# Performance work log

Measured on AMD Instinct MI355X. Metric: run time of the kernel, lower is better.

## Reference

```python
import jax, jax.numpy as jnp
import numpy as np

EMBED_DIM = 1024
HEADS = 16
HEAD_DIM = EMBED_DIM // HEADS


def setup_inputs() -> dict:
    key = jax.random.key(0)
    ks = jax.random.split(key, 9)
    B, T, C = 4, 4096, EMBED_DIM
    s = 1.0 / np.sqrt(C)
    inp = {
        "x": jax.random.normal(ks[0], (B, T, C), dtype=jnp.float32),
        "Wq": jax.random.normal(ks[1], (C, C), dtype=jnp.float32) * s,
        "bq": jnp.zeros((C,), dtype=jnp.float32),
        "Wk": jax.random.normal(ks[2], (C, C), dtype=jnp.float32) * s,
        "bk": jnp.zeros((C,), dtype=jnp.float32),
        "Wv": jax.random.normal(ks[3], (C, C), dtype=jnp.float32) * s,
        "bv": jnp.zeros((C,), dtype=jnp.float32),
        "Wc": jax.random.normal(ks[4], (C, C), dtype=jnp.float32) * s,
        "bc": jnp.zeros((C,), dtype=jnp.float32),
    }
    return inp


def reference(x, Wq, bq, Wk, bk, Wv, bv, Wc, bc):
    B, T, C = x.shape
    H, D = HEADS, HEAD_DIM
    # projections (torch Linear: x @ W.T + b)
    q = (x @ Wq.T + bq).reshape(B, T, H, D).transpose(0, 2, 1, 3)  # [B,H,T,D]
    k = (x @ Wk.T + bk).reshape(B, T, H, D).transpose(0, 2, 1, 3)
    v = (x @ Wv.T + bv).reshape(B, T, H, D).transpose(0, 2, 1, 3)
    # ELU+1 feature map
    q = jax.nn.elu(q) + 1.0
    k = jax.nn.elu(k) + 1.0
    # kv outer product: [B,H,D,D]
    kv = jnp.einsum("bhtd,bhte->bhde", k, v)
    # normalizer: q @ sum_t k  -> [B,H,T,1]
    k_sum = k.sum(axis=2)  # [B,H,D]
    z = 1.0 / (jnp.einsum("bhtd,bhd->bht", q, k_sum)[..., None] + 1e-6)
    y = jnp.einsum("bhtd,bhde->bhte", q, kv) * z  # [B,H,T,D]
    y = y.transpose(0, 2, 1, 3).reshape(B, T, C)
    return y @ Wc.T + bc
```

## Files before the change

### kernel.cpp

```cpp
#include <hip/hip_runtime.h>
#include <math.h>

#define EMBED 1024
#define HEADS 16
#define HD 64
#define BATCH 4
#define TSEQ 4096
#define BH (BATCH * HEADS)
#define MROWS (BATCH * TSEQ)

typedef _Float16 f16;
typedef __attribute__((ext_vector_type(4))) _Float16 f16x4;
typedef __attribute__((ext_vector_type(8))) _Float16 f16x8;
typedef __attribute__((ext_vector_type(4))) float f32x4;

#define GLOBAL_AS __attribute__((address_space(1)))
#define LDS_AS __attribute__((address_space(3)))

__device__ __forceinline__ float elu1(float v) {
    return v > 0.f ? v + 1.f : __expf(v);
}

__device__ __forceinline__ int swzc(int row, int col, int cols) {
    int g = (col >> 3) ^ (row & 7);
    return row * cols + (g << 3) + (col & 7);
}

__device__ __forceinline__ f16x8 fragld(const f16* t, int row, int k, int cols) {
    return *(const f16x8*)&t[swzc(row, k, cols)];
}

__device__ __forceinline__ f32x4 mfma16(f16x8 a, f16x8 b, f32x4 c) {
    return __builtin_amdgcn_mfma_f32_16x16x32_f16(a, b, c, 0, 0, 0);
}

__device__ __forceinline__ void gld_lds16(const f16* g, f16* l) {
    __builtin_amdgcn_global_load_lds((const GLOBAL_AS void*)g, (LDS_AS void*)l, 16, 0, 0);
}

__global__ __launch_bounds__(256) void prep(
    const float* __restrict__ x, f16* __restrict__ xh,
    const float* __restrict__ Wq, const float* __restrict__ Wk,
    const float* __restrict__ Wv, const float* __restrict__ Wc,
    const float* __restrict__ bq, const float* __restrict__ bk,
    const float* __restrict__ bv, const float* __restrict__ bc,
    f16* __restrict__ Wall, float* __restrict__ ball, float* __restrict__ kvz)
{
    int bid = blockIdx.x;
    if (bid < 16384) {
        size_t i4 = (size_t)bid * 256 + threadIdx.x;
        float4 f = *(const float4*)&x[i4 * 4];
        f16x4 h = {(f16)f.x, (f16)f.y, (f16)f.z, (f16)f.w};
        *(f16x4*)&xh[i4 * 4] = h;
    } else {
        int i4 = (bid - 16384) * 256 + threadIdx.x;
        int cls = i4 >> 18;
        const float* W = cls == 0 ? Wq : cls == 1 ? Wk : cls == 2 ? Wv : Wc;
        int off = (i4 & 0x3FFFF) * 4;
        float4 f = *(const float4*)&W[off];
        f16x4 h = {(f16)f.x, (f16)f.y, (f16)f.z, (f16)f.w};
        *(f16x4*)&Wall[(size_t)i4 * 4] = h;
        if (i4 < 4096) {
            int c2 = i4 >> 10;
            const float* bb = c2 == 0 ? bq : c2 == 1 ? bk : c2 == 2 ? bv : bc;
            ball[i4] = bb[i4 & 1023];
        }
        if (i4 < 66560) {
            *(float4*)&kvz[i4 * 4] = (float4){0.f, 0.f, 0.f, 0.f};
        }
    }
}

__global__ __launch_bounds__(256) void gemm_qkv(
    const f16* __restrict__ xh, const f16* __restrict__ Wall,
    const float* __restrict__ ball,
    f16* __restrict__ q, float* __restrict__ kvg, float* __restrict__ ksg)
{
    __shared__ __align__(16) f16 smem[2 * 128 * 64];
    f16* As = smem;
    f16* Bs = smem + 128 * 64;

    const int tid = threadIdx.x, lane = tid & 63, w = tid >> 6;
    const int wr = w >> 1, wc4 = w & 1, l15 = lane & 15, l4 = lane >> 4;

    const int m0 = blockIdx.x * 128;
    const int ny = blockIdx.y;
    const bool isq = (ny < 8);
    const int h = ny - 8;

    const int gcol = ((lane & 7) ^ (lane >> 3)) << 3;
    const int rsub = lane >> 3;
    const size_t arow = (size_t)(m0 + w * 32 + rsub) * EMBED + gcol;

    const int wrow = w * 32 + rsub;
    int brow_idx;
    if (isq)          brow_idx = ny * 128 + wrow;
    else if (wrow < 64) brow_idx = 1024 + h * 64 + wrow;
    else                brow_idx = 2048 + h * 64 + (wrow - 64);
    const size_t brow = (size_t)brow_idx * EMBED + gcol;

    f32x4 acc[4][4];
    #pragma unroll
    for (int i = 0; i < 4; ++i)
        #pragma unroll
        for (int j = 0; j < 4; ++j) acc[i][j] = (f32x4){0.f, 0.f, 0.f, 0.f};

    for (int k0 = 0; k0 < EMBED; k0 += 64) {
        #pragma unroll
        for (int c = 0; c < 4; ++c) {
            gld_lds16(&xh[arow + (size_t)c * 8 * EMBED + k0], &As[(w * 4 + c) * 512]);
            gld_lds16(&Wall[brow + (size_t)c * 8 * EMBED + k0], &Bs[(w * 4 + c) * 512]);
        }
        __syncthreads();
        #pragma unroll
        for (int kk = 0; kk < 64; kk += 32) {
            f16x8 af[4], bf[4];
            #pragma unroll
            for (int i = 0; i < 4; ++i)
                af[i] = fragld(As, wr * 64 + i * 16 + l15, kk + l4 * 8, 64);
            #pragma unroll
            for (int j = 0; j < 4; ++j)
                bf[j] = fragld(Bs, wc4 * 64 + j * 16 + l15, kk + l4 * 8, 64);
            #pragma unroll
            for (int i = 0; i < 4; ++i)
                #pragma unroll
                for (int j = 0; j < 4; ++j)
                    acc[i][j] = mfma16(af[i], bf[j], acc[i][j]);
        }
        __syncthreads();
    }

    if (isq) {
        const int n0 = ny * 128;
        #pragma unroll
        for (int j = 0; j < 4; ++j) {
            int c = wc4 * 64 + j * 16 + l15;
            float bj = ball[n0 + c];
            #pragma unroll
            for (int i = 0; i < 4; ++i) {
                #pragma unroll
                for (int r = 0; r < 4; ++r) {
                    int t = wr * 64 + i * 16 + l4 * 4 + r;
                    smem[swzc(t, c, 128)] = (f16)elu1(acc[i][j][r] + bj);
                }
            }
        }
        __syncthreads();
        #pragma unroll
        for (int p = 0; p < 8; ++p) {
            int idx = tid + p * 256;
            int row = idx >> 4, g8 = (idx & 15) << 3;
            f16x8 v = *(const f16x8*)&smem[swzc(row, g8, 128)];
            *(f16x8*)&q[(size_t)(m0 + row) * EMBED + n0 + g8] = v;
        }
    } else {
        f16* kt = As;
        f16* vt = Bs;
        const float* biasp = ball + (wc4 ? 2048 : 1024) + h * 64;
        #pragma unroll
        for (int j = 0; j < 4; ++j) {
            int d = j * 16 + l15;
            float bj = biasp[d];
            f16* dst = wc4 ? vt : kt;
            #pragma unroll
            for (int i = 0; i < 4; ++i) {
                int t0 = wr * 64 + i * 16 + l4 * 4;
                f16x4 hv;
                #pragma unroll
                for (int r = 0; r < 4; ++r) {
                    float vv = acc[i][j][r] + bj;
                    if (!wc4) vv = elu1(vv);
                    hv[r] = (f16)vv;
                }
                *(f16x4*)&dst[swzc(d, t0, 128)] = hv;
            }
        }
        __syncthreads();

        f32x4 kvacc[4];
        #pragma unroll
        for (int j = 0; j < 4; ++j) kvacc[j] = (f32x4){0.f, 0.f, 0.f, 0.f};
        #pragma unroll
        for (int tc = 0; tc < 4; ++tc) {
            f16x8 a = fragld(vt, 16 * w + l15, tc * 32 + l4 * 8, 128);
            #pragma unroll
            for (int j = 0; j < 4; ++j) {
                f16x8 bfr = fragld(kt, j * 16 + l15, tc * 32 + l4 * 8, 128);
                kvacc[j] = mfma16(a, bfr, kvacc[j]);
            }
        }
        float ksacc = 0.f;
        {
            int d = tid & 63, q4 = tid >> 6;
            #pragma unroll
            for (int t8 = 0; t8 < 32; t8 += 8) {
                f16x8 k8 = fragld(kt, d, q4 * 32 + t8, 128);
                #pragma unroll
                for (int e = 0; e < 8; ++e) ksacc += (float)k8[e];
            }
        }
        const int bh = (m0 >> 12) * HEADS + h;
        #pragma unroll
        for (int j = 0; j < 4; ++j)
            #pragma unroll
            for (int r = 0; r < 4; ++r)
                atomicAdd(&kvg[(size_t)bh * 4096 +
                               (size_t)(16 * w + l4 * 4 + r) * HD + j * 16 + l15],
                          kvacc[j][r]);
        atomicAdd(&ksg[bh * HD + (tid & 63)], ksacc);
    }
}

__global__ __launch_bounds__(256) void y_kernel(
    const f16* __restrict__ q, const float* __restrict__ kvg,
    const float* __restrict__ ksg, f16* __restrict__ y)
{
    __shared__ __align__(16) f16 qs[128 * 64];
    __shared__ __align__(16) f16 kvs[64 * 64];
    __shared__ __align__(16) f16 ylds[128 * 64];
    __shared__ float kss[64];
    __shared__ float zs[128];

    const int bh = blockIdx.x, b = bh >> 4, h = bh & 15;
    const int tid = threadIdx.x, lane = tid & 63, w = tid >> 6;
    const int l15 = lane & 15, l4 = lane >> 4;
    const int t0g = b * TSEQ + blockIdx.y * 128;

    #pragma unroll
    for (int c = 0; c < 4; ++c) {
        int idx = tid + c * 256;
        int row = idx >> 3, col8 = (idx & 7) << 3;
        f16x8 v = *(const f16x8*)&q[(size_t)(t0g + row) * EMBED + h * 64 + col8];
        *(f16x8*)&qs[swzc(row, col8, 64)] = v;
    }
    #pragma unroll
    for (int c = 0; c < 4; ++c) {
        int idx = tid + c * 256;
        int e = idx >> 4, d4 = (idx & 15) << 2;
        float4 f = *(const float4*)&kvg[(size_t)bh * 4096 + e * 64 + d4];
        f16x4 hv = {(f16)f.x, (f16)f.y, (f16)f.z, (f16)f.w};
        *(f16x4*)&kvs[swzc(e, d4, 64)] = hv;
    }
    if (tid < 64) kss[tid] = ksg[bh * HD + tid];
    __syncthreads();

    {
        int t = tid >> 1, dh = (tid & 1) * 32;
        float s = 0.f;
        #pragma unroll
        for (int d8 = 0; d8 < 32; d8 += 8) {
            f16x8 qv = fragld(qs, t, dh + d8, 64);
            #pragma unroll
            for (int e = 0; e < 8; ++e) s += (float)qv[e] * kss[dh + d8 + e];
        }
        s += __shfl_xor(s, 1);
        if ((tid & 1) == 0) zs[t] = 1.f / (s + 1e-6f);
    }
    __syncthreads();

    f32x4 yacc[8];
    #pragma unroll
    for (int jn = 0; jn < 8; ++jn) yacc[jn] = (f32x4){0.f, 0.f, 0.f, 0.f};
    #pragma unroll
    for (int kk = 0; kk < 64; kk += 32) {
        f16x8 a = fragld(kvs, 16 * w + l15, kk + l4 * 8, 64);
        #pragma unroll
        for (int jn = 0; jn < 8; ++jn) {
            f16x8 bq8 = fragld(qs, jn * 16 + l15, kk + l4 * 8, 64);
            yacc[jn] = mfma16(a, bq8, yacc[jn]);
        }
    }
    #pragma unroll
    for (int jn = 0; jn < 8; ++jn) {
        int t = jn * 16 + l15;
        float z = zs[t];
        int e0 = 16 * w + l4 * 4;
        f16x4 hv;
        #pragma unroll
        for (int r = 0; r < 4; ++r) hv[r] = (f16)(yacc[jn][r] * z);
        *(f16x4*)&ylds[swzc(t, e0, 64)] = hv;
    }
    __syncthreads();

    {
        int row = tid >> 1, eh = (tid & 1) * 32;
        size_t gb = (size_t)(t0g + row) * EMBED + h * 64 + eh;
        #pragma unroll
        for (int c8 = 0; c8 < 32; c8 += 8) {
            f16x8 v = fragld(ylds, row, eh + c8, 64);
            *(f16x8*)&y[gb + c8] = v;
        }
    }
}

__global__ __launch_bounds__(256) void gemm_out(
    const f16* __restrict__ y, const f16* __restrict__ Wall,
    const float* __restrict__ ball, float* __restrict__ out)
{
    __shared__ __align__(16) f16 As[128 * 64];
    __shared__ __align__(16) f16 Bs[128 * 64];

    const int tid = threadIdx.x, lane = tid & 63, w = tid >> 6;
    const int wr = w >> 1, wc4 = w & 1, l15 = lane & 15, l4 = lane >> 4;
    const int m0 = blockIdx.x * 128;
    const int n0 = blockIdx.y * 128;

    const int gcol = ((lane & 7) ^ (lane >> 3)) << 3;
    const int rsub = lane >> 3;
    const size_t arow = (size_t)(m0 + w * 32 + rsub) * EMBED + gcol;
    const size_t brow = (size_t)(3072 + n0 + w * 32 + rsub) * EMBED + gcol;

    f32x4 acc[4][4];
    #pragma unroll
    for (int i = 0; i < 4; ++i)
        #pragma unroll
        for (int j = 0; j < 4; ++j) acc[i][j] = (f32x4){0.f, 0.f, 0.f, 0.f};

    for (int k0 = 0; k0 < EMBED; k0 += 64) {
        #pragma unroll
        for (int c = 0; c < 4; ++c) {
            gld_lds16(&y[arow + (size_t)c * 8 * EMBED + k0], &As[(w * 4 + c) * 512]);
            gld_lds16(&Wall[brow + (size_t)c * 8 * EMBED + k0], &Bs[(w * 4 + c) * 512]);
        }
        __syncthreads();
        #pragma unroll
        for (int kk = 0; kk < 64; kk += 32) {
            f16x8 af[4], bf[4];
            #pragma unroll
            for (int i = 0; i < 4; ++i)
                af[i] = fragld(As, wr * 64 + i * 16 + l15, kk + l4 * 8, 64);
            #pragma unroll
            for (int j = 0; j < 4; ++j)
                bf[j] = fragld(Bs, wc4 * 64 + j * 16 + l15, kk + l4 * 8, 64);
            #pragma unroll
            for (int i = 0; i < 4; ++i)
                #pragma unroll
                for (int j = 0; j < 4; ++j)
                    acc[i][j] = mfma16(af[i], bf[j], acc[i][j]);
        }
        __syncthreads();
    }

    #pragma unroll
    for (int j = 0; j < 4; ++j) {
        int n = n0 + wc4 * 64 + j * 16 + l15;
        float bj = ball[3072 + n];
        #pragma unroll
        for (int i = 0; i < 4; ++i) {
            #pragma unroll
            for (int r = 0; r < 4; ++r) {
                int m = m0 + wr * 64 + i * 16 + l4 * 4 + r;
                out[(size_t)m * EMBED + n] = acc[i][j][r] + bj;
            }
        }
    }
}

extern "C" void kernel_launch(void* const* d_in, const int* in_sizes, int n_in,
                              void* d_out, int out_size, void* d_ws, size_t ws_size,
                              hipStream_t stream) {
    (void)in_sizes; (void)n_in; (void)out_size; (void)ws_size;
    const float* x  = (const float*)d_in[0];
    const float* Wq = (const float*)d_in[1];
    const float* bq = (const float*)d_in[2];
    const float* Wk = (const float*)d_in[3];
    const float* bk = (const float*)d_in[4];
    const float* Wv = (const float*)d_in[5];
    const float* bv = (const float*)d_in[6];
    const float* Wc = (const float*)d_in[7];
    const float* bc = (const float*)d_in[8];
    float* out = (float*)d_out;

    char* W = (char*)d_ws;
    f16* xh   = (f16*)W;
    f16* q_ws = (f16*)(W + 33554432);
    f16* Wall = (f16*)(W + 67108864);
    float* ball = (float*)(W + 75497472);
    float* kvg  = (float*)(W + 75513856);
    float* ksg  = (float*)(W + 76562432);

    prep<<<20480, 256, 0, stream>>>(x, xh, Wq, Wk, Wv, Wc, bq, bk, bv, bc,
                                    Wall, ball, kvg);

    gemm_qkv<<<dim3(128, 24), 256, 0, stream>>>(xh, Wall, ball, q_ws, kvg, ksg);

    y_kernel<<<dim3(BH, TSEQ / 128), 256, 0, stream>>>(q_ws, kvg, ksg, q_ws);

    gemm_out<<<dim3(128, 8), 256, 0, stream>>>(q_ws, Wall, ball, out);
}
```

Baseline: 226.2 us.

## Split KV projection from Q projection and fuse Q GEMM with y computation

The combined QKV GEMM becomes two kernels. The first computes only K/V and accumulates kv and k_sum with atomics. The second computes the Q projection tile and then applies ELU+1, the normalizer and the kv product in the epilogue for the two heads covered by each 128-column tile, writing y directly. This removes the q round-trip through global memory and the separate y_kernel launch. In exchange the Q GEMM now must wait until all K/V work finishes, and the fused epilogue adds LDS traffic and register pressure.

```diff
diff --git a/kernel.cpp b/kernel.cpp
--- a/kernel.cpp
+++ b/kernel.cpp
@@ -71,10 +71,10 @@
     }
 }
 
-__global__ __launch_bounds__(256) void gemm_qkv(
+__global__ __launch_bounds__(256) void gemm_kv(
     const f16* __restrict__ xh, const f16* __restrict__ Wall,
     const float* __restrict__ ball,
-    f16* __restrict__ q, float* __restrict__ kvg, float* __restrict__ ksg)
+    float* __restrict__ kvg, float* __restrict__ ksg)
 {
     __shared__ __align__(16) f16 smem[2 * 128 * 64];
     f16* As = smem;
@@ -84,19 +84,15 @@
     const int wr = w >> 1, wc4 = w & 1, l15 = lane & 15, l4 = lane >> 4;
 
     const int m0 = blockIdx.x * 128;
-    const int ny = blockIdx.y;
-    const bool isq = (ny < 8);
-    const int h = ny - 8;
+    const int h = blockIdx.y;
 
     const int gcol = ((lane & 7) ^ (lane >> 3)) << 3;
     const int rsub = lane >> 3;
     const size_t arow = (size_t)(m0 + w * 32 + rsub) * EMBED + gcol;
 
     const int wrow = w * 32 + rsub;
-    int brow_idx;
-    if (isq)          brow_idx = ny * 128 + wrow;
-    else if (wrow < 64) brow_idx = 1024 + h * 64 + wrow;
-    else                brow_idx = 2048 + h * 64 + (wrow - 64);
+    const int brow_idx = (wrow < 64) ? (1024 + h * 64 + wrow)
+                                     : (2048 + h * 64 + (wrow - 64));
     const size_t brow = (size_t)brow_idx * EMBED + gcol;
 
     f32x4 acc[4][4];
@@ -130,166 +126,199 @@
         __syncthreads();
     }
 
-    if (isq) {
-        const int n0 = ny * 128;
+    f16* kt = As;
+    f16* vt = Bs;
+    const float* biasp = ball + (wc4 ? 2048 : 1024) + h * 64;
+    #pragma unroll
+    for (int j = 0; j < 4; ++j) {
+        int d = j * 16 + l15;
+        float bj = biasp[d];
+        f16* dst = wc4 ? vt : kt;
+        #pragma unroll
+        for (int i = 0; i < 4; ++i) {
+            int t0 = wr * 64 + i * 16 + l4 * 4;
+            f16x4 hv;
+            #pragma unroll
+            for (int r = 0; r < 4; ++r) {
+                float vv = acc[i][j][r] + bj;
+                if (!wc4) vv = elu1(vv);
+                hv[r] = (f16)vv;
+            }
+            *(f16x4*)&dst[swzc(d, t0, 128)] = hv;
+        }
+    }
+    __syncthreads();
+
+    f32x4 kvacc[4];
+    #pragma unroll
+    for (int j = 0; j < 4; ++j) kvacc[j] = (f32x4){0.f, 0.f, 0.f, 0.f};
+    #pragma unroll
+    for (int tc = 0; tc < 4; ++tc) {
+        f16x8 a = fragld(vt, 16 * w + l15, tc * 32 + l4 * 8, 128);
         #pragma unroll
         for (int j = 0; j < 4; ++j) {
-            int c = wc4 * 64 + j * 16 + l15;
-            float bj = ball[n0 + c];
-            #pragma unroll
-            for (int i = 0; i < 4; ++i) {
+            f16x8 bfr = fragld(kt, j * 16 + l15, tc * 32 + l4 * 8, 128);
+            kvacc[j] = mfma16(a, bfr, kvacc[j]);
+        }
+    }
+    float ksacc = 0.f;
+    {
+        int d = tid & 63, q4 = tid >> 6;
+        #pragma unroll
+        for (int t8 = 0; t8 < 32; t8 += 8) {
+            f16x8 k8 = fragld(kt, d, q4 * 32 + t8, 128);
+            #pragma unroll
+            for (int e = 0; e < 8; ++e) ksacc += (float)k8[e];
+        }
+    }
+    const int bh = (m0 >> 12) * HEADS + h;
+    #pragma unroll
+    for (int j = 0; j < 4; ++j)
+        #pragma unroll
+        for (int r = 0; r < 4; ++r)
+            atomicAdd(&kvg[(size_t)bh * 4096 +
+                           (size_t)(16 * w + l4 * 4 + r) * HD + j * 16 + l15],
+                      kvacc[j][r]);
+    atomicAdd(&ksg[bh * HD + (tid & 63)], ksacc);
+}
+
+__global__ __launch_bounds__(256) void gemm_qy(
+    const f16* __restrict__ xh, const f16* __restrict__ Wall,
+    const float* __restrict__ ball,
+    const float* __restrict__ kvg, const float* __restrict__ ksg,
+    f16* __restrict__ y)
+{
+    __shared__ __align__(16) f16 smem[2 * 128 * 64];
+    __shared__ __align__(16) f16 kvs[2][64 * 64];
+    __shared__ float kss[2][64];
+    __shared__ float zs[128][2];
+    f16* As = smem;
+    f16* Bs = smem + 128 * 64;
+
+    const int tid = threadIdx.x, lane = tid & 63, w = tid >> 6;
+    const int wr = w >> 1, wc4 = w & 1, l15 = lane & 15, l4 = lane >> 4;
+
+    const int m0 = blockIdx.x * 128;
+    const int ny = blockIdx.y;
+    const int n0 = ny * 128;
+    const int bh0 = (m0 >> 12) * HEADS + 2 * ny;
+
+    const int gcol = ((lane & 7) ^ (lane >> 3)) << 3;
+    const int rsub = lane >> 3;
+    const size_t arow = (size_t)(m0 + w * 32 + rsub) * EMBED + gcol;
+    const size_t brow = (size_t)(n0 + w * 32 + rsub) * EMBED + gcol;
+
+    f32x4 acc[4][4];
+    #pragma unroll
+    for (int i = 0; i < 4; ++i)
+        #pragma unroll
+        for (int j = 0; j < 4; ++j) acc[i][j] = (f32x4){0.f, 0.f, 0.f, 0.f};
+
+    for (int k0 = 0; k0 < EMBED; k0 += 64) {
+        #pragma unroll
+        for (int c = 0; c < 4; ++c) {
+            gld_lds16(&xh[arow + (size_t)c * 8 * EMBED + k0], &As[(w * 4 + c) * 512]);
+            gld_lds16(&Wall[brow + (size_t)c * 8 * EMBED + k0], &Bs[(w * 4 + c) * 512]);
+        }
+        __syncthreads();
+        #pragma unroll
+        for (int kk = 0; kk < 64; kk += 32) {
+            f16x8 af[4], bf[4];
+            #pragma unroll
+            for (int i = 0; i < 4; ++i)
+                af[i] = fragld(As, wr * 64 + i * 16 + l15, kk + l4 * 8, 64);
+            #pragma unroll
+            for (int j = 0; j < 4; ++j)
+                bf[j] = fragld(Bs, wc4 * 64 + j * 16 + l15, kk + l4 * 8, 64);
+            #pragma unroll
+            for (int i = 0; i < 4; ++i)
                 #pragma unroll
-                for (int r = 0; r < 4; ++r) {
-                    int t = wr * 64 + i * 16 + l4 * 4 + r;
-                    smem[swzc(t, c, 128)] = (f16)elu1(acc[i][j][r] + bj);
-                }
+                for (int j = 0; j < 4; ++j)
+                    acc[i][j] = mfma16(af[i], bf[j], acc[i][j]);
+        }
+        __syncthreads();
+    }
+
+    #pragma unroll
+    for (int c = 0; c < 8; ++c) {
+        int idx = tid + c * 256;
+        int hh = idx >> 10;
+        int rem = idx & 1023;
+        int e = rem >> 4, d4 = (rem & 15) << 2;
+        float4 f = *(const float4*)&kvg[(size_t)(bh0 + hh) * 4096 + e * 64 + d4];
+        f16x4 hv = {(f16)f.x, (f16)f.y, (f16)f.z, (f16)f.w};
+        *(f16x4*)&kvs[hh][swzc(e, d4, 64)] = hv;
+    }
+    if (tid < 128) kss[tid >> 6][tid & 63] = ksg[(bh0 + (tid >> 6)) * HD + (tid & 63)];
+
+    #pragma unroll
+    for (int j = 0; j < 4; ++j) {
+        int c = wc4 * 64 + j * 16 + l15;
+        float bj = ball[n0 + c];
+        #pragma unroll
+        for (int i = 0; i < 4; ++i) {
+            #pragma unroll
+            for (int r = 0; r < 4; ++r) {
+                int t = wr * 64 + i * 16 + l4 * 4 + r;
+                smem[swzc(t, c, 128)] = (f16)elu1(acc[i][j][r] + bj);
             }
         }
-        __syncthreads();
-        #pragma unroll
-        for (int p = 0; p < 8; ++p) {
-            int idx = tid + p * 256;
-            int row = idx >> 4, g8 = (idx & 15) << 3;
-            f16x8 v = *(const f16x8*)&smem[swzc(row, g8, 128)];
-            *(f16x8*)&q[(size_t)(m0 + row) * EMBED + n0 + g8] = v;
-        }
-    } else {
-        f16* kt = As;
-        f16* vt = Bs;
-        const float* biasp = ball + (wc4 ? 2048 : 1024) + h * 64;
-        #pragma unroll
-        for (int j = 0; j < 4; ++j) {
-            int d = j * 16 + l15;
-            float bj = biasp[d];
-            f16* dst = wc4 ? vt : kt;
-            #pragma unroll
-            for (int i = 0; i < 4; ++i) {
-                int t0 = wr * 64 + i * 16 + l4 * 4;
-                f16x4 hv;
-                #pragma unroll
-                for (int r = 0; r < 4; ++r) {
-                    float vv = acc[i][j][r] + bj;
-                    if (!wc4) vv = elu1(vv);
-                    hv[r] = (f16)vv;
-                }
-                *(f16x4*)&dst[swzc(d, t0, 128)] = hv;
-            }
-        }
-        __syncthreads();
-
-        f32x4 kvacc[4];
-        #pragma unroll
-        for (int j = 0; j < 4; ++j) kvacc[j] = (f32x4){0.f, 0.f, 0.f, 0.f};
-        #pragma unroll
-        for (int tc = 0; tc < 4; ++tc) {
-            f16x8 a = fragld(vt, 16 * w + l15, tc * 32 + l4 * 8, 128);
-            #pragma unroll
-            for (int j = 0; j < 4; ++j) {
-                f16x8 bfr = fragld(kt, j * 16 + l15, tc * 32 + l4 * 8, 128);
-                kvacc[j] = mfma16(a, bfr, kvacc[j]);
-            }
-        }
-        float ksacc = 0.f;
-        {
-            int d = tid & 63, q4 = tid >> 6;
-            #pragma unroll
-            for (int t8 = 0; t8 < 32; t8 += 8) {
-                f16x8 k8 = fragld(kt, d, q4 * 32 + t8, 128);
-                #pragma unroll
-                for (int e = 0; e < 8; ++e) ksacc += (float)k8[e];
-            }
-        }
-        const int bh = (m0 >> 12) * HEADS + h;
-        #pragma unroll
-        for (int j = 0; j < 4; ++j)
-            #pragma unroll
-            for (int r = 0; r < 4; ++r)
-                atomicAdd(&kvg[(size_t)bh * 4096 +
-                               (size_t)(16 * w + l4 * 4 + r) * HD + j * 16 + l15],
-                          kvacc[j][r]);
-        atomicAdd(&ksg[bh * HD + (tid & 63)], ksacc);
-    }
-}
-
-__global__ __launch_bounds__(256) void y_kernel(
-    const f16* __restrict__ q, const float* __restrict__ kvg,
-    const float* __restrict__ ksg, f16* __restrict__ y)
-{
-    __shared__ __align__(16) f16 qs[128 * 64];
-    __shared__ __align__(16) f16 kvs[64 * 64];
-    __shared__ __align__(16) f16 ylds[128 * 64];
-    __shared__ float kss[64];
-    __shared__ float zs[128];
-
-    const int bh = blockIdx.x, b = bh >> 4, h = bh & 15;
-    const int tid = threadIdx.x, lane = tid & 63, w = tid >> 6;
-    const int l15 = lane & 15, l4 = lane >> 4;
-    const int t0g = b * TSEQ + blockIdx.y * 128;
-
-    #pragma unroll
-    for (int c = 0; c < 4; ++c) {
-        int idx = tid + c * 256;
-        int row = idx >> 3, col8 = (idx & 7) << 3;
-        f16x8 v = *(const f16x8*)&q[(size_t)(t0g + row) * EMBED + h * 64 + col8];
-        *(f16x8*)&qs[swzc(row, col8, 64)] = v;
-    }
-    #pragma unroll
-    for (int c = 0; c < 4; ++c) {
-        int idx = tid + c * 256;
-        int e = idx >> 4, d4 = (idx & 15) << 2;
-        float4 f = *(const float4*)&kvg[(size_t)bh * 4096 + e * 64 + d4];
-        f16x4 hv = {(f16)f.x, (f16)f.y, (f16)f.z, (f16)f.w};
-        *(f16x4*)&kvs[swzc(e, d4, 64)] = hv;
-    }
-    if (tid < 64) kss[tid] = ksg[bh * HD + tid];
+    }
     __syncthreads();
 
     {
-        int t = tid >> 1, dh = (tid & 1) * 32;
+        int t = tid >> 1, hh = tid & 1;
         float s = 0.f;
         #pragma unroll
-        for (int d8 = 0; d8 < 32; d8 += 8) {
-            f16x8 qv = fragld(qs, t, dh + d8, 64);
-            #pragma unroll
-            for (int e = 0; e < 8; ++e) s += (float)qv[e] * kss[dh + d8 + e];
-        }
-        s += __shfl_xor(s, 1);
-        if ((tid & 1) == 0) zs[t] = 1.f / (s + 1e-6f);
+        for (int d8 = 0; d8 < 64; d8 += 8) {
+            f16x8 qv = fragld(smem, t, hh * 64 + d8, 128);
+            #pragma unroll
+            for (int e = 0; e < 8; ++e) s += (float)qv[e] * kss[hh][d8 + e];
+        }
+        zs[t][hh] = 1.f / (s + 1e-6f);
+    }
+
+    const int hh = w >> 1;
+    const int eh = (w & 1) * 32;
+    f32x4 yacc[2][8];
+    #pragma unroll
+    for (int et = 0; et < 2; ++et)
+        #pragma unroll
+        for (int jn = 0; jn < 8; ++jn) yacc[et][jn] = (f32x4){0.f, 0.f, 0.f, 0.f};
+    #pragma unroll
+    for (int kk = 0; kk < 64; kk += 32) {
+        f16x8 a0 = fragld(kvs[hh], eh + l15, kk + l4 * 8, 64);
+        f16x8 a1 = fragld(kvs[hh], eh + 16 + l15, kk + l4 * 8, 64);
+        #pragma unroll
+        for (int jn = 0; jn < 8; ++jn) {
+            f16x8 bq8 = fragld(smem, jn * 16 + l15, hh * 64 + kk + l4 * 8, 128);
+            yacc[0][jn] = mfma16(a0, bq8, yacc[0][jn]);
+            yacc[1][jn] = mfma16(a1, bq8, yacc[1][jn]);
+        }
     }
     __syncthreads();
 
-    f32x4 yacc[8];
-    #pragma unroll
-    for (int jn = 0; jn < 8; ++jn) yacc[jn] = (f32x4){0.f, 0.f, 0.f, 0.f};
-    #pragma unroll
-    for (int kk = 0; kk < 64; kk += 32) {
-        f16x8 a = fragld(kvs, 16 * w + l15, kk + l4 * 8, 64);
+    #pragma unroll
+    for (int et = 0; et < 2; ++et) {
         #pragma unroll
         for (int jn = 0; jn < 8; ++jn) {
-            f16x8 bq8 = fragld(qs, jn * 16 + l15, kk + l4 * 8, 64);
-            yacc[jn] = mfma16(a, bq8, yacc[jn]);
-        }
-    }
-    #pragma unroll
-    for (int jn = 0; jn < 8; ++jn) {
-        int t = jn * 16 + l15;
-        float z = zs[t];
-        int e0 = 16 * w + l4 * 4;
-        f16x4 hv;
-        #pragma unroll
-        for (int r = 0; r < 4; ++r) hv[r] = (f16)(yacc[jn][r] * z);
-        *(f16x4*)&ylds[swzc(t, e0, 64)] = hv;
+            int t = jn * 16 + l15;
+            float z = zs[t][hh];
+            int c0 = hh * 64 + eh + et * 16 + l4 * 4;
+            f16x4 hv;
+            #pragma unroll
+            for (int r = 0; r < 4; ++r) hv[r] = (f16)(yacc[et][jn][r] * z);
+            *(f16x4*)&smem[swzc(t, c0, 128)] = hv;
+        }
     }
     __syncthreads();
 
-    {
-        int row = tid >> 1, eh = (tid & 1) * 32;
-        size_t gb = (size_t)(t0g + row) * EMBED + h * 64 + eh;
-        #pragma unroll
-        for (int c8 = 0; c8 < 32; c8 += 8) {
-            f16x8 v = fragld(ylds, row, eh + c8, 64);
-            *(f16x8*)&y[gb + c8] = v;
-        }
+    #pragma unroll
+    for (int p = 0; p < 8; ++p) {
+        int idx = tid + p * 256;
+        int row = idx >> 4, g8 = (idx & 15) << 3;
+        f16x8 v = *(const f16x8*)&smem[swzc(row, g8, 128)];
+        *(f16x8*)&y[(size_t)(m0 + row) * EMBED + n0 + g8] = v;
     }
 }
 
@@ -373,7 +402,7 @@
 
     char* W = (char*)d_ws;
     f16* xh   = (f16*)W;
-    f16* q_ws = (f16*)(W + 33554432);
+    f16* y_ws = (f16*)(W + 33554432);
     f16* Wall = (f16*)(W + 67108864);
     float* ball = (float*)(W + 75497472);
     float* kvg  = (float*)(W + 75513856);
@@ -382,9 +411,9 @@
     prep<<<20480, 256, 0, stream>>>(x, xh, Wq, Wk, Wv, Wc, bq, bk, bv, bc,
                                     Wall, ball, kvg);
 
-    gemm_qkv<<<dim3(128, 24), 256, 0, stream>>>(xh, Wall, ball, q_ws, kvg, ksg);
-
-    y_kernel<<<dim3(BH, TSEQ / 128), 256, 0, stream>>>(q_ws, kvg, ksg, q_ws);
-
-    gemm_out<<<dim3(128, 8), 256, 0, stream>>>(q_ws, Wall, ball, out);
-}
+    gemm_kv<<<dim3(128, 16), 256, 0, stream>>>(xh, Wall, ball, kvg, ksg);
+
+    gemm_qy<<<dim3(128, 8), 256, 0, stream>>>(xh, Wall, ball, kvg, ksg, y_ws);
+
+    gemm_out<<<dim3(128, 8), 256, 0, stream>>>(y_ws, Wall, ball, out);
+}
```

After: 216.6 us (median of 2 runs). 1.04x faster.
